# Performance work log

Measured on AMD Instinct MI355X. Metric: run time of the kernel, lower is better.

The kernel has to match this reference:

```python
import jax, jax.numpy as jnp
import numpy as np

DIM = 1024; SD = 1024; N_BANDS = 4; MIMO_P = 8; BATCH = 2; L = 2048
LOG10000 = float(np.log(10000.0))


def _hippo_freqs(sd):
    n = jnp.arange(sd, dtype=jnp.float32)
    f = jnp.sqrt(2.0 * n + 1.0)
    f = f / f[-1]
    return jnp.exp(-f * LOG10000)


def setup_inputs() -> dict:
    key = jax.random.key(0)
    ks = jax.random.split(key, 16)
    dim, sd = DIM, SD
    wscale = 1.0 / np.sqrt(dim)
    n = jnp.arange(sd, dtype=jnp.float32)
    b0 = jnp.sqrt(2.0 * n + 1.0); b0 = b0 / b0[-1]
    b0_inv = jnp.log(jnp.expm1(jnp.clip(b0, 1e-6, None)))  # softplus^-1 of hippo b
    G = sd // MIMO_P
    inp = dict(
        x=jax.random.normal(ks[0], (BATCH, L, dim), jnp.float32),
        z_prev=jax.random.normal(ks[1], (BATCH, L, dim), jnp.float32),
        W_psi=jax.random.normal(ks[2], (2 * sd, dim), jnp.float32) * wscale,
        b_psi=jnp.zeros(2 * sd, jnp.float32),
        W_phi=jax.random.normal(ks[3], (2 * sd, dim), jnp.float32) * wscale,
        b_phi=jnp.zeros(2 * sd, jnp.float32),
        W_gate=jax.random.normal(ks[4], (1, dim), jnp.float32) * wscale,
        b_gate=jnp.zeros(1, jnp.float32),
        surprise_gain=jnp.zeros(1, jnp.float32),
        omega=_hippo_freqs(sd),
        log_gamma=jax.random.normal(ks[5], (sd,), jnp.float32) * 0.5 - 7.0,
        dt=jnp.float32(np.log(np.expm1(0.1))),  # layer_idx=0, depth=1 -> target_dt=0.1
        W_bs=jax.random.normal(ks[6], (sd, dim), jnp.float32) * 0.02,
        b_bs=b0_inv,
        W_ps=jax.random.uniform(ks[7], (sd, dim), jnp.float32, -wscale, wscale),
        b_ps=jnp.zeros(sd, jnp.float32),
        W_btx=jax.random.normal(ks[8], (sd, dim), jnp.float32) * 0.02,
        b_btx=b0_inv,
        W_bth=jax.random.normal(ks[9], (sd, 2 * sd), jnp.float32) * 0.02,
        b_bth=jnp.zeros(sd, jnp.float32),
        W_ptx=jax.random.uniform(ks[10], (sd, dim), jnp.float32, -wscale, wscale),
        b_ptx=jnp.zeros(sd, jnp.float32),
        mimo_w=jnp.eye(MIMO_P, dtype=jnp.float32)[None].repeat(G, 0)
               + 0.02 * jax.random.normal(ks[11], (G, MIMO_P, MIMO_P), jnp.float32),
        tau=jnp.ones(1, jnp.float32),
        beta=jnp.zeros(1, jnp.float32),
    )
    return inp


def _forward(x, z_prev, W_psi, b_psi, W_phi, b_phi, W_gate, b_gate, surprise_gain,
             omega, log_gamma, dt, W_bs, b_bs, W_ps, b_ps, W_btx, b_btx,
             W_bth, b_bth, W_ptx, b_ptx, mimo_w, tau, beta):
    Bsz, Ls, D = x.shape
    sd = omega.shape[0]
    n_fft = 1 << (2 * Ls - 1).bit_length()  # static

    # unitary mask: band 0 = lowest hippo frequencies (slowest modes) stay lossless
    freqs = _hippo_freqs(sd)
    order = jnp.argsort(freqs)
    band0 = order[: sd // N_BANDS]
    not_unitary = jnp.ones(sd, jnp.float32).at[band0].set(0.0)

    lin = lambda a, W, bb: a @ W.T + bb

    psi_raw = lin(x, W_psi, b_psi)
    psi = jax.lax.complex(psi_raw[..., :sd], psi_raw[..., sd:])
    phi_raw = lin(x, W_phi, b_phi)
    phi = jax.lax.complex(phi_raw[..., :sd], phi_raw[..., sd:])

    gate = jax.nn.sigmoid(lin(x, W_gate, b_gate))  # [B,L,1]
    surprise = jnp.mean(jnp.abs(x - z_prev), -1, keepdims=True)
    gate = gate * (1.0 + jnp.tanh(surprise_gain) * surprise)

    dt_eff = jax.nn.softplus(dt)
    gamma_eff = jax.nn.softplus(log_gamma) * not_unitary
    lam = jax.lax.complex(-gamma_eff, omega)  # [SD]
    t = jnp.arange(Ls, dtype=jnp.float32)
    kernel_raw = jnp.exp(lam[None, :] * (t[:, None] * dt_eff))  # [L,SD] A^t
    k_pad = jnp.concatenate([jnp.zeros((2, sd), kernel_raw.dtype), kernel_raw], 0)
    kernel_simpson = (k_pad[2:] + 4.0 * k_pad[1:-1] + k_pad[:-2]) / 6.0  # Simpson taps

    Kf_scout = jnp.fft.fft(kernel_raw.T, n=n_fft, axis=1)      # [SD,n_fft]
    Kf_true = jnp.fft.fft(kernel_simpson.T, n=n_fft, axis=1)

    def fftconv(U, Kf):  # causal conv via FFT: U [B,L,SD] complex
        Uf = jnp.fft.fft(jnp.transpose(U, (0, 2, 1)), n=n_fft, axis=2)
        H = jnp.fft.ifft(Uf * Kf[None], axis=2)[:, :, :Ls]
        return jnp.transpose(H, (0, 2, 1))

    # ---- scout wave: input-only LTI ----
    b_scout = jax.nn.softplus(lin(x, W_bs, b_bs))
    ph_s = jnp.pi * jnp.tanh(lin(x, W_ps, b_ps))
    Bc_s = jax.lax.complex(b_scout * jnp.cos(ph_s), b_scout * jnp.sin(ph_s))
    U_scout = gate * Bc_s * psi
    H_scout = fftconv(U_scout, Kf_scout)
    H_prev = jnp.pad(H_scout, ((0, 0), (1, 0), (0, 0)))[:, :-1]  # shift by 1
    scout_rms = jnp.sqrt(jnp.mean(H_prev.real ** 2 + H_prev.imag ** 2, -1, keepdims=True) + 1e-6)
    Hn = H_prev / scout_rms
    H_flat = jnp.concatenate([Hn.real, Hn.imag], -1)  # [B,L,2SD]

    # ---- true wave: state-dependent B, Simpson quadrature kernel ----
    b_true = jax.nn.softplus(lin(x, W_btx, b_btx) + lin(H_flat, W_bth, b_bth))
    ph_t = jnp.pi * jnp.tanh(lin(x, W_ptx, b_ptx))
    Bc_t = jax.lax.complex(b_true * jnp.cos(ph_t), b_true * jnp.sin(ph_t))
    U_true = gate * Bc_t * psi
    H = fftconv(U_true, Kf_true)

    read_rms = jnp.sqrt(jnp.mean(H.real ** 2 + H.imag ** 2, -1, keepdims=True) + 1e-6)
    Hn2 = H / read_rms

    # block-diagonal MIMO mixing in groups of mimo_p
    G = sd // MIMO_P
    Hg = Hn2.reshape(Bsz, Ls, G, MIMO_P)
    Hm = jnp.einsum('blgp,gpq->blgq', Hg, mimo_w.astype(Hg.dtype)).reshape(Bsz, Ls, sd)

    # Born-rule measurement: out = Re(h * phi^*), affine read temperature
    out = jnp.real(Hm * jnp.conj(phi))
    return tau * out + beta  # SD == dim -> out_proj is Identity


def reference(x, z_prev, W_psi, b_psi, W_phi, b_phi, W_gate, b_gate, surprise_gain,
              omega, log_gamma, dt, W_bs, b_bs, W_ps, b_ps, W_btx, b_btx,
              W_bth, b_bth, W_ptx, b_ptx, mimo_w, tau, beta):
    return _forward(x, z_prev, W_psi, b_psi, W_phi, b_phi, W_gate, b_gate,
                    surprise_gain, omega, log_gamma, dt, W_bs, b_bs, W_ps, b_ps,
                    W_btx, b_btx, W_bth, b_bth, W_ptx, b_ptx, mimo_w, tau, beta)
```

## Files before the change

### kernel.cpp

```cpp
#include <hip/hip_runtime.h>
#include <math.h>

#define DIMX   1024
#define SDN    1024
#define BATCHN 2
#define LSEQ   2048
#define BLROWS (BATCHN*LSEQ)
#define NCHUNK 128
#define LCHUNK (LSEQ/NCHUNK)
#define PI_F   3.14159265358979f

typedef unsigned short ushort_t;
typedef unsigned int uint_t;
typedef __bf16 bf16_t;
typedef bf16_t bf16x8 __attribute__((ext_vector_type(8)));
typedef float f32x4 __attribute__((ext_vector_type(4)));

__device__ __forceinline__ ushort_t f2bf_rne(float f) {
  unsigned u = __float_as_uint(f);
  u = u + 0x7fffu + ((u >> 16) & 1u);
  return (ushort_t)(u >> 16);
}

__device__ __forceinline__ float bf2f(ushort_t u) {
  return __uint_as_float(((unsigned)u) << 16);
}

__device__ __forceinline__ uint_t pk2(float2 v) {
  return (uint_t)f2bf_rne(v.x) | ((uint_t)f2bf_rne(v.y) << 16);
}
__device__ __forceinline__ float2 upk2(uint_t u) {
  return make_float2(__uint_as_float(u << 16), __uint_as_float(u & 0xffff0000u));
}

__device__ __forceinline__ float2 cfma2(float2 a, float2 v, float2 u) {
  float re = fmaf(a.x, v.x, fmaf(-a.y, v.y, u.x));
  float im = fmaf(a.x, v.y, fmaf(a.y, v.x, u.y));
  return make_float2(re, im);
}
__device__ __forceinline__ float2 cmul2(float2 a, float2 b) {
  return make_float2(a.x * b.x - a.y * b.y, a.x * b.y + a.y * b.x);
}

__device__ __forceinline__ float fast_softplus(float x) {
  return x > 15.f ? x : __logf(1.f + __expf(x));
}
__device__ __forceinline__ float fast_tanh(float x) {
  float xc = fminf(fmaxf(x, -9.f), 9.f);
  float t = __expf(2.f * xc);
  return (t - 1.f) * __builtin_amdgcn_rcpf(t + 1.f);
}

__device__ __forceinline__ void gload_lds16(const ushort_t* g, ushort_t* l) {
  __builtin_amdgcn_global_load_lds(
      (const __attribute__((address_space(1))) void*)g,
      (__attribute__((address_space(3))) void*)l, 16, 0, 0);
}

__global__ __launch_bounds__(256) void prep_kernel(
    const float* __restrict__ x, const float* __restrict__ z_prev,
    const float* __restrict__ Wpsi, const float* __restrict__ Wphi,
    const float* __restrict__ Wbs, const float* __restrict__ Wps,
    const float* __restrict__ Wbtx, const float* __restrict__ Wptx,
    const float* __restrict__ Wbth,
    const float* __restrict__ b_psi, const float* __restrict__ b_phi,
    const float* __restrict__ b_bs, const float* __restrict__ b_ps,
    const float* __restrict__ b_btx, const float* __restrict__ b_ptx,
    const float* __restrict__ Wg, const float* __restrict__ bg,
    const float* __restrict__ sg,
    const float* __restrict__ omega, const float* __restrict__ log_gamma,
    const float* __restrict__ dt,
    ushort_t* __restrict__ xb, ushort_t* __restrict__ wcat,
    ushort_t* __restrict__ wbthb, float* __restrict__ bcat,
    float* __restrict__ gate, float2* __restrict__ a_out,
    float2* __restrict__ A_out) {
  int b = blockIdx.x;
  int tid = threadIdx.x;
  if (b < 4096) {
    int i = tid * 4;
    const float* xp = x + (size_t)b * DIMX;
    const float* zp = z_prev + (size_t)b * DIMX;
    float4 xv = *(const float4*)(xp + i);
    float4 zv = *(const float4*)(zp + i);
    float4 wv = *(const float4*)(Wg + i);
    ushort4 o;
    o.x = f2bf_rne(xv.x); o.y = f2bf_rne(xv.y);
    o.z = f2bf_rne(xv.z); o.w = f2bf_rne(xv.w);
    *(ushort4*)(xb + (size_t)b * DIMX + i) = o;
    float dot = xv.x * wv.x + xv.y * wv.y + xv.z * wv.z + xv.w * wv.w;
    float sur = fabsf(xv.x - zv.x) + fabsf(xv.y - zv.y) +
                fabsf(xv.z - zv.z) + fabsf(xv.w - zv.w);
    __shared__ float sdot[256], ssur[256];
    sdot[tid] = dot; ssur[tid] = sur;
    __syncthreads();
    for (int o_ = 128; o_ > 0; o_ >>= 1) {
      if (tid < o_) { sdot[tid] += sdot[tid + o_]; ssur[tid] += ssur[tid + o_]; }
      __syncthreads();
    }
    if (tid == 0) {
      float gs = 1.f / (1.f + expf(-(sdot[0] + bg[0])));
      gate[b] = gs * (1.f + tanhf(sg[0]) * (ssur[0] * (1.f / DIMX)));
    }
    return;
  }
  b -= 4096;
  if (b < 10240) {
    const float* src; ushort_t* dst; int off;
    if (b < 2048)       { src = Wpsi; dst = wcat;             off = b; }
    else if (b < 4096)  { src = Wphi; dst = wcat + 2097152u;  off = b - 2048; }
    else if (b < 5120)  { src = Wbs;  dst = wcat + 4194304u;  off = b - 4096; }
    else if (b < 6144)  { src = Wps;  dst = wcat + 5242880u;  off = b - 5120; }
    else if (b < 7168)  { src = Wbtx; dst = wcat + 6291456u;  off = b - 6144; }
    else if (b < 8192)  { src = Wptx; dst = wcat + 7340032u;  off = b - 7168; }
    else                { src = Wbth; dst = wbthb;            off = b - 8192; }
    int i = (off * 256 + tid) * 4;
    float4 v = *(const float4*)(src + i);
    ushort4 o;
    o.x = f2bf_rne(v.x); o.y = f2bf_rne(v.y);
    o.z = f2bf_rne(v.z); o.w = f2bf_rne(v.w);
    *(ushort4*)(dst + i) = o;
    return;
  }
  b -= 10240;
  if (b < 32) {
    int n = b * 256 + tid;
    float v;
    if (n < 2048) v = b_psi[n];
    else if (n < 4096) v = b_phi[n - 2048];
    else if (n < 5120) v = b_bs[n - 4096];
    else if (n < 6144) v = b_ps[n - 5120];
    else if (n < 7168) v = b_btx[n - 6144];
    else v = b_ptx[n - 7168];
    bcat[n] = v;
    return;
  }
  int s = (b - 32) * 256 + tid;
  double dtv = (double)dt[0];
  double dte = dtv > 20.0 ? dtv : log1p(exp(dtv));
  double gam = 0.0;
  if (s < SDN - SDN / 4) {
    double lg = (double)log_gamma[s];
    gam = lg > 20.0 ? lg : log1p(exp(lg));
  }
  double th = (double)omega[s] * dte;
  double r  = exp(-gam * dte);
  a_out[s] = make_float2((float)(r * cos(th)), (float)(r * sin(th)));
  double thl = th * (double)LCHUNK;
  double rl  = exp(-gam * dte * (double)LCHUNK);
  A_out[s] = make_float2((float)(rl * cos(thl)), (float)(rl * sin(thl)));
}

template<int MODE>
__global__ __launch_bounds__(256, 2) void gemm_bf16(
    const ushort_t* __restrict__ Xb, const ushort_t* __restrict__ Wb,
    const float* __restrict__ bias, ushort_t* __restrict__ Cb) {
  __shared__ ushort_t As[2][4096];
  __shared__ ushort_t Bs[2][4096];
  const int tid = threadIdx.x;
  const int w = tid >> 6, l = tid & 63;
  int bm, bn, ldx, ldw;
  const ushort_t *Xp, *Wp;
  if (MODE == 0) {
    int b = blockIdx.x;
    int xcd = b & 7, idx = b >> 3;
    int tx = ((xcd & 3) << 4) + (idx & 15);
    int ty = ((xcd >> 2) << 4) + (idx >> 4);
    bm = ty << 7; bn = tx << 7;
    ldx = 1024; ldw = 1024;
    Xp = Xb; Wp = Wb;
  } else {
    bm = blockIdx.y << 7; bn = blockIdx.x << 7;
    ldx = 2048; ldw = 2048;
    Xp = Xb + blockIdx.z * 1024;
    Wp = Wb + blockIdx.z * 1024;
  }
  const int wr = w >> 1, wc = w & 1;

  const int srow = tid >> 2;
  const int c8 = (((tid & 3) - (tid >> 3)) & 3) << 3;
  const ushort_t* ga0 = Xp + (size_t)(bm + srow) * ldx + c8;
  const ushort_t* ga1 = Xp + (size_t)(bm + 64 + srow) * ldx + c8;
  const ushort_t* gb0 = Wp + (size_t)(bn + srow) * ldw + c8;
  const ushort_t* gb1 = Wp + (size_t)(bn + 64 + srow) * ldw + c8;

  f32x4 acc[4][4] = {};
  const int nk = 32;

#define STAGE(buf, kt)                                   \
  do {                                                   \
    gload_lds16(ga0 + (kt), &As[buf][w * 512]);          \
    gload_lds16(ga1 + (kt), &As[buf][2048 + w * 512]);   \
    gload_lds16(gb0 + (kt), &Bs[buf][w * 512]);          \
    gload_lds16(gb1 + (kt), &Bs[buf][2048 + w * 512]);   \
  } while (0)

  STAGE(0, 0);
  __syncthreads();

  const int rl = l & 15, kh = l >> 4;
  const int chunkp = (kh + (rl >> 1)) & 3;
  for (int kt = 0; kt < nk; ++kt) {
    int cur = kt & 1;
    if (kt + 1 < nk) STAGE(cur ^ 1, (kt + 1) * 32);
    const uint4* Af = (const uint4*)As[cur];
    const uint4* Bf = (const uint4*)Bs[cur];
    bf16x8 a[4], b[4];
#pragma unroll
    for (int i = 0; i < 4; ++i)
      a[i] = __builtin_bit_cast(bf16x8, Af[(wr * 64 + i * 16 + rl) * 4 + chunkp]);
#pragma unroll
    for (int j = 0; j < 4; ++j)
      b[j] = __builtin_bit_cast(bf16x8, Bf[(wc * 64 + j * 16 + rl) * 4 + chunkp]);
#pragma unroll
    for (int i = 0; i < 4; ++i)
#pragma unroll
      for (int j = 0; j < 4; ++j)
        acc[i][j] = __builtin_amdgcn_mfma_f32_16x16x32_bf16(a[i], b[j], acc[i][j], 0, 0, 0);
    __syncthreads();
  }
#undef STAGE

#pragma unroll
  for (int i = 0; i < 4; ++i) {
    int mrow = bm + wr * 64 + i * 16 + (l >> 4) * 4;
#pragma unroll
    for (int j = 0; j < 4; ++j) {
      int ncol = bn + wc * 64 + j * 16 + (l & 15);
      if (MODE == 0) {
        float bv = bias[ncol];
#pragma unroll
        for (int r = 0; r < 4; ++r)
          Cb[(size_t)(mrow + r) * 8192 + ncol] = f2bf_rne(acc[i][j][r] + bv);
      } else {
        ushort_t* P = Cb + (size_t)blockIdx.z * (4096u * 1024u);
#pragma unroll
        for (int r = 0; r < 4; ++r)
          P[(size_t)(mrow + r) * 1024 + ncol] = f2bf_rne(acc[i][j][r]);
      }
    }
  }
}


__global__ __launch_bounds__(256) void u_scout(
    const float* __restrict__ gate, const ushort_t* __restrict__ proj,
    uint_t* __restrict__ U) {
  int idx2 = blockIdx.x * 256 + threadIdx.x;
  int m = idx2 >> 9, sp = (idx2 & 511) << 1;
  const ushort_t* pr = proj + ((size_t)m << 13);
  float g = gate[m];
  uint_t bsu = *(const uint_t*)(pr + 4096 + sp);
  uint_t psu = *(const uint_t*)(pr + 5120 + sp);
  uint_t pre = *(const uint_t*)(pr + sp);
  uint_t pim = *(const uint_t*)(pr + 1024 + sp);
  uint_t o[2];
#pragma unroll
  for (int e = 0; e < 2; ++e) {
    float bv = fast_softplus(bf2f((ushort_t)(e ? (bsu >> 16) : (bsu & 0xffff))));
    float ph = PI_F * fast_tanh(bf2f((ushort_t)(e ? (psu >> 16) : (psu & 0xffff))));
    float sph, cph;
    __sincosf(ph, &sph, &cph);
    float br = bv * cph, bi = bv * sph;
    float prf = bf2f((ushort_t)(e ? (pre >> 16) : (pre & 0xffff)));
    float pif = bf2f((ushort_t)(e ? (pim >> 16) : (pim & 0xffff)));
    o[e] = pk2(make_float2(g * (br * prf - bi * pif), g * (br * pif + bi * prf)));
  }
  *(uint2*)(U + ((size_t)m << 10) + sp) = make_uint2(o[0], o[1]);
}

__global__ __launch_bounds__(256) void u_true(
    const float* __restrict__ gate, const ushort_t* __restrict__ proj,
    const ushort_t* __restrict__ P0, const ushort_t* __restrict__ P1,
    const float* __restrict__ b_bth, uint_t* __restrict__ U) {
  int idx2 = blockIdx.x * 256 + threadIdx.x;
  int m = idx2 >> 9, sp = (idx2 & 511) << 1;
  const ushort_t* pr = proj + ((size_t)m << 13);
  float g = gate[m];
  size_t base = ((size_t)m << 10) + sp;
  uint_t btu = *(const uint_t*)(pr + 6144 + sp);
  uint_t ptu = *(const uint_t*)(pr + 7168 + sp);
  uint_t p0u = *(const uint_t*)(P0 + base);
  uint_t p1u = *(const uint_t*)(P1 + base);
  float2 bb = *(const float2*)(b_bth + sp);
  uint_t pre = *(const uint_t*)(pr + sp);
  uint_t pim = *(const uint_t*)(pr + 1024 + sp);
  uint_t o[2];
#pragma unroll
  for (int e = 0; e < 2; ++e) {
    float blv = bf2f((ushort_t)(e ? (btu >> 16) : (btu & 0xffff)))
              + bf2f((ushort_t)(e ? (p0u >> 16) : (p0u & 0xffff)))
              + bf2f((ushort_t)(e ? (p1u >> 16) : (p1u & 0xffff)))
              + (e ? bb.y : bb.x);
    float bv = fast_softplus(blv);
    float ph = PI_F * fast_tanh(bf2f((ushort_t)(e ? (ptu >> 16) : (ptu & 0xffff))));
    float sph, cph;
    __sincosf(ph, &sph, &cph);
    float br = bv * cph, bi = bv * sph;
    float prf = bf2f((ushort_t)(e ? (pre >> 16) : (pre & 0xffff)));
    float pif = bf2f((ushort_t)(e ? (pim >> 16) : (pim & 0xffff)));
    o[e] = pk2(make_float2(g * (br * prf - bi * pif), g * (br * pif + bi * prf)));
  }
  *(uint2*)(U + base) = make_uint2(o[0], o[1]);
}

__global__ __launch_bounds__(256) void scan_stage1(
    const uint_t* __restrict__ U, const float2* __restrict__ a,
    float2* __restrict__ carry) {
  int s = blockIdx.x * 256 + threadIdx.x;
  int c = blockIdx.y, b = blockIdx.z;
  float2 av = a[s];
  float2 V = make_float2(0.f, 0.f);
  const uint_t* Up = U + (size_t)(b * LSEQ + c * LCHUNK) * SDN + s;
#pragma unroll 8
  for (int t = 0; t < LCHUNK; ++t)
    V = cfma2(av, V, upk2(Up[(size_t)t * SDN]));
  carry[(size_t)(b * NCHUNK + c) * SDN + s] = V;
}

__global__ __launch_bounds__(256) void scan_stage2(
    const float2* __restrict__ carry, const float2* __restrict__ Ac,
    float2* __restrict__ prefix) {
  int tid = threadIdx.x;
  int lane = tid & 63;
  int s = blockIdx.x * 4 + (tid >> 6);
  int b = blockIdx.z;
  float2 Av = Ac[s];
  size_t base0 = (size_t)(b * NCHUNK + 2 * lane) * SDN + s;
  float2 c0 = carry[base0];
  float2 c1 = carry[base0 + SDN];
  float2 x = cfma2(Av, c0, c1);
  float2 M = cmul2(Av, Av);
#pragma unroll
  for (int sh = 1; sh < 64; sh <<= 1) {
    float2 y;
    y.x = __shfl_up(x.x, sh, 64);
    y.y = __shfl_up(x.y, sh, 64);
    if (lane >= sh) x = cfma2(M, y, x);
    M = cmul2(M, M);
  }
  float2 p0;
  p0.x = __shfl_up(x.x, 1, 64);
  p0.y = __shfl_up(x.y, 1, 64);
  if (lane == 0) p0 = make_float2(0.f, 0.f);
  float2 p1 = cfma2(Av, p0, c0);
  prefix[base0] = p0;
  prefix[base0 + SDN] = p1;
}

__global__ __launch_bounds__(256) void scan_stage3(
    const uint_t* __restrict__ U, const float2* __restrict__ a,
    const float2* __restrict__ prefix, uint_t* __restrict__ Vout) {
  int s = blockIdx.x * 256 + threadIdx.x;
  int c = blockIdx.y, b = blockIdx.z;
  float2 av = a[s];
  float2 V = prefix[(size_t)(b * NCHUNK + c) * SDN + s];
  size_t base = (size_t)(b * LSEQ + c * LCHUNK) * SDN + s;
#pragma unroll 8
  for (int t = 0; t < LCHUNK; ++t) {
    V = cfma2(av, V, upk2(U[base + (size_t)t * SDN]));
    Vout[base + (size_t)t * SDN] = pk2(V);
  }
}

__global__ __launch_bounds__(256) void hflat_kernel(
    const uint_t* __restrict__ V, ushort_t* __restrict__ Hflat) {
  int m = blockIdx.x;
  int t = m & (LSEQ - 1);
  float2 v[4];
  float sum = 0.f;
#pragma unroll
  for (int i = 0; i < 4; ++i) {
    int s = threadIdx.x + i * 256;
    float2 vv = make_float2(0.f, 0.f);
    if (t > 0) vv = upk2(V[(size_t)(m - 1) * SDN + s]);
    v[i] = vv;
    sum += vv.x * vv.x + vv.y * vv.y;
  }
  __shared__ float red[256];
  red[threadIdx.x] = sum;
  __syncthreads();
  for (int o = 128; o > 0; o >>= 1) {
    if (threadIdx.x < o) red[threadIdx.x] += red[threadIdx.x + o];
    __syncthreads();
  }
  float inv = 1.0f / sqrtf(red[0] * (1.f / SDN) + 1e-6f);
  ushort_t* hr = Hflat + ((size_t)m << 11);
#pragma unroll
  for (int i = 0; i < 4; ++i) {
    int s = threadIdx.x + i * 256;
    hr[s] = f2bf_rne(v[i].x * inv);
    hr[SDN + s] = f2bf_rne(v[i].y * inv);
  }
}

__global__ __launch_bounds__(256) void final_kernel(
    const uint_t* __restrict__ V, const ushort_t* __restrict__ proj,
    const float* __restrict__ mimo, const float* __restrict__ tau,
    const float* __restrict__ beta, float* __restrict__ out) {
  int bid = blockIdx.x;
  int m = ((bid & 7) << 9) | (bid >> 3);
  int t = m & (LSEQ - 1);
  __shared__ float2 hl[SDN];
  __shared__ float red[256];
  float sum = 0.f;
#pragma unroll
  for (int i = 0; i < 4; ++i) {
    int s = threadIdx.x + i * 256;
    float2 v0 = upk2(V[(size_t)m * SDN + s]);
    float2 v1 = make_float2(0.f, 0.f), v2 = make_float2(0.f, 0.f);
    if (t >= 1) v1 = upk2(V[(size_t)(m - 1) * SDN + s]);
    if (t >= 2) v2 = upk2(V[(size_t)(m - 2) * SDN + s]);
    float2 h = make_float2((v0.x + 4.f * v1.x + v2.x) * (1.f / 6.f),
                           (v0.y + 4.f * v1.y + v2.y) * (1.f / 6.f));
    hl[s] = h;
    sum += h.x * h.x + h.y * h.y;
  }
  red[threadIdx.x] = sum;
  __syncthreads();
  for (int o = 128; o > 0; o >>= 1) {
    if (threadIdx.x < o) red[threadIdx.x] += red[threadIdx.x + o];
    __syncthreads();
  }
  float inv = 1.0f / sqrtf(red[0] * (1.f / SDN) + 1e-6f);
  float tv = tau[0], bv = beta[0];
  const ushort_t* pp = proj + ((size_t)m << 13) + 2048;
#pragma unroll
  for (int i = 0; i < 4; ++i) {
    int s = threadIdx.x + i * 256;
    int g = s >> 3, q = s & 7;
    const float* wp = mimo + (size_t)g * 64 + q;
    float hr = 0.f, hi = 0.f;
#pragma unroll
    for (int p = 0; p < 8; ++p) {
      float wv = wp[p * 8];
      float2 hp = hl[(g << 3) + p];
      hr = fmaf(hp.x, wv, hr);
      hi = fmaf(hp.y, wv, hi);
    }
    hr *= inv; hi *= inv;
    float o1 = hr * bf2f(pp[s]) + hi * bf2f(pp[SDN + s]);
    out[(size_t)m * SDN + s] = tv * o1 + bv;
  }
}

extern "C" void kernel_launch(void* const* d_in, const int* in_sizes, int n_in,
                              void* d_out, int out_size, void* d_ws, size_t ws_size,
                              hipStream_t stream) {
  const float* x      = (const float*)d_in[0];
  const float* z_prev = (const float*)d_in[1];
  const float* W_psi  = (const float*)d_in[2];
  const float* b_psi  = (const float*)d_in[3];
  const float* W_phi  = (const float*)d_in[4];
  const float* b_phi  = (const float*)d_in[5];
  const float* W_gate = (const float*)d_in[6];
  const float* b_gate = (const float*)d_in[7];
  const float* s_gain = (const float*)d_in[8];
  const float* omega  = (const float*)d_in[9];
  const float* log_g  = (const float*)d_in[10];
  const float* dt     = (const float*)d_in[11];
  const float* W_bs   = (const float*)d_in[12];
  const float* b_bs   = (const float*)d_in[13];
  const float* W_ps   = (const float*)d_in[14];
  const float* b_ps   = (const float*)d_in[15];
  const float* W_btx  = (const float*)d_in[16];
  const float* b_btx  = (const float*)d_in[17];
  const float* W_bth  = (const float*)d_in[18];
  const float* b_bth  = (const float*)d_in[19];
  const float* W_ptx  = (const float*)d_in[20];
  const float* b_ptx  = (const float*)d_in[21];
  const float* mimo_w = (const float*)d_in[22];
  const float* tau    = (const float*)d_in[23];
  const float* beta   = (const float*)d_in[24];
  float* out = (float*)d_out;

  float* ws = (float*)d_ws;
  const size_t M1 = 1 << 20;
  ushort_t* proj   = (ushort_t*)ws;
  uint_t*   U      = (uint_t*)(ws + 16 * M1);
  uint_t*   V      = U;
  ushort_t* xb     = (ushort_t*)(ws + 24 * M1);
  ushort_t* wcat   = (ushort_t*)(ws + 26 * M1);
  ushort_t* P0     = wcat;
  ushort_t* P1     = wcat + 4u * 1024u * 1024u;
  ushort_t* wbthb  = (ushort_t*)(ws + 30 * M1);
  ushort_t* hflatB = (ushort_t*)(ws + 31 * M1);
  float*    bcat   = ws + 35 * M1;
  float*    gate   = bcat + 8192;
  float2*   ac     = (float2*)(gate + 4096);
  float2*   Ac     = ac + 1024;
  float2*   carry  = Ac + 1024;
  float2*   prefix = carry + 262144;
  (void)ws_size; (void)in_sizes; (void)n_in; (void)out_size;

  dim3 blk(256);
  dim3 sgrid(SDN / 256, NCHUNK, BATCHN);
  dim3 s2grid(SDN / 4, 1, BATCHN);

  prep_kernel<<<dim3(14372), blk, 0, stream>>>(
      x, z_prev, W_psi, W_phi, W_bs, W_ps, W_btx, W_ptx, W_bth,
      b_psi, b_phi, b_bs, b_ps, b_btx, b_ptx,
      W_gate, b_gate, s_gain, omega, log_g, dt,
      xb, wcat, wbthb, bcat, gate, ac, Ac);

  gemm_bf16<0><<<dim3(2048), blk, 0, stream>>>(xb, wcat, bcat, proj);

  u_scout<<<dim3(BLROWS * SDN / 512), blk, 0, stream>>>(gate, proj, U);
  scan_stage1<<<sgrid, blk, 0, stream>>>(U, ac, carry);
  scan_stage2<<<s2grid, blk, 0, stream>>>(carry, Ac, prefix);
  scan_stage3<<<sgrid, blk, 0, stream>>>(U, ac, prefix, V);

  hflat_kernel<<<dim3(BLROWS), blk, 0, stream>>>(V, hflatB);
  gemm_bf16<1><<<dim3(8, 32, 2), blk, 0, stream>>>(hflatB, wbthb, bcat, P0);

  u_true<<<dim3(BLROWS * SDN / 512), blk, 0, stream>>>(gate, proj, P0, P1, b_bth, U);
  scan_stage1<<<sgrid, blk, 0, stream>>>(U, ac, carry);
  scan_stage2<<<s2grid, blk, 0, stream>>>(carry, Ac, prefix);
  scan_stage3<<<sgrid, blk, 0, stream>>>(U, ac, prefix, V);

  final_kernel<<<dim3(BLROWS), blk, 0, stream>>>(V, proj, mimo_w, tau, beta, out);
}
```

Baseline: 202.5 us.

## Fuse three-stage chunked scan into one cooperative kernel with grid syncs

Replaces the three separate scan kernels (chunk carry, carry prefix, chunk rescan) with a single cooperative launch that uses grid-wide barriers between the phases. The middle phase reuses the first 512 blocks of the same grid. This removes two kernel launches and their inter-kernel gaps per scan, of which there are two in the forward pass. The grid is 1024 blocks of 256 threads, which must all be co-resident for the cooperative launch, and grid.sync adds its own barrier cost.

```diff
diff --git a/kernel.cpp b/kernel.cpp
--- a/kernel.cpp
+++ b/kernel.cpp
@@ -1,5 +1,8 @@
 #include <hip/hip_runtime.h>
+#include <hip/hip_cooperative_groups.h>
 #include <math.h>
+
+namespace cg = cooperative_groups;
 
 #define DIMX   1024
 #define SDN    1024
@@ -303,62 +306,62 @@
   *(uint2*)(U + base) = make_uint2(o[0], o[1]);
 }
 
-__global__ __launch_bounds__(256) void scan_stage1(
-    const uint_t* __restrict__ U, const float2* __restrict__ a,
-    float2* __restrict__ carry) {
-  int s = blockIdx.x * 256 + threadIdx.x;
-  int c = blockIdx.y, b = blockIdx.z;
-  float2 av = a[s];
-  float2 V = make_float2(0.f, 0.f);
-  const uint_t* Up = U + (size_t)(b * LSEQ + c * LCHUNK) * SDN + s;
+__global__ __launch_bounds__(256) void scan_fused(
+    uint_t* __restrict__ U, const float2* __restrict__ a,
+    const float2* __restrict__ Ac, float2* __restrict__ carry,
+    float2* __restrict__ prefix) {
+  cg::grid_group grid = cg::this_grid();
+  const int tid = threadIdx.x;
+  const int s = blockIdx.x * 256 + tid;
+  const int c = blockIdx.y, b = blockIdx.z;
+  const float2 av = a[s];
+  {
+    float2 V = make_float2(0.f, 0.f);
+    const uint_t* Up = U + (size_t)(b * LSEQ + c * LCHUNK) * SDN + s;
 #pragma unroll 8
-  for (int t = 0; t < LCHUNK; ++t)
-    V = cfma2(av, V, upk2(Up[(size_t)t * SDN]));
-  carry[(size_t)(b * NCHUNK + c) * SDN + s] = V;
-}
-
-__global__ __launch_bounds__(256) void scan_stage2(
-    const float2* __restrict__ carry, const float2* __restrict__ Ac,
-    float2* __restrict__ prefix) {
-  int tid = threadIdx.x;
-  int lane = tid & 63;
-  int s = blockIdx.x * 4 + (tid >> 6);
-  int b = blockIdx.z;
-  float2 Av = Ac[s];
-  size_t base0 = (size_t)(b * NCHUNK + 2 * lane) * SDN + s;
-  float2 c0 = carry[base0];
-  float2 c1 = carry[base0 + SDN];
-  float2 x = cfma2(Av, c0, c1);
-  float2 M = cmul2(Av, Av);
-#pragma unroll
-  for (int sh = 1; sh < 64; sh <<= 1) {
-    float2 y;
-    y.x = __shfl_up(x.x, sh, 64);
-    y.y = __shfl_up(x.y, sh, 64);
-    if (lane >= sh) x = cfma2(M, y, x);
-    M = cmul2(M, M);
-  }
-  float2 p0;
-  p0.x = __shfl_up(x.x, 1, 64);
-  p0.y = __shfl_up(x.y, 1, 64);
-  if (lane == 0) p0 = make_float2(0.f, 0.f);
-  float2 p1 = cfma2(Av, p0, c0);
-  prefix[base0] = p0;
-  prefix[base0 + SDN] = p1;
-}
-
-__global__ __launch_bounds__(256) void scan_stage3(
-    const uint_t* __restrict__ U, const float2* __restrict__ a,
-    const float2* __restrict__ prefix, uint_t* __restrict__ Vout) {
-  int s = blockIdx.x * 256 + threadIdx.x;
-  int c = blockIdx.y, b = blockIdx.z;
-  float2 av = a[s];
-  float2 V = prefix[(size_t)(b * NCHUNK + c) * SDN + s];
-  size_t base = (size_t)(b * LSEQ + c * LCHUNK) * SDN + s;
+    for (int t = 0; t < LCHUNK; ++t)
+      V = cfma2(av, V, upk2(Up[(size_t)t * SDN]));
+    carry[(size_t)(b * NCHUNK + c) * SDN + s] = V;
+  }
+  grid.sync();
+  {
+    int fid = (blockIdx.z * NCHUNK + blockIdx.y) * (SDN / 256) + blockIdx.x;
+    if (fid < 512) {
+      int lane = tid & 63;
+      int s2 = (fid & 255) * 4 + (tid >> 6);
+      int b2 = fid >> 8;
+      float2 Av = Ac[s2];
+      size_t base0 = (size_t)(b2 * NCHUNK + 2 * lane) * SDN + s2;
+      float2 c0 = carry[base0];
+      float2 c1 = carry[base0 + SDN];
+      float2 x = cfma2(Av, c0, c1);
+      float2 M = cmul2(Av, Av);
+#pragma unroll
+      for (int sh = 1; sh < 64; sh <<= 1) {
+        float2 y;
+        y.x = __shfl_up(x.x, sh, 64);
+        y.y = __shfl_up(x.y, sh, 64);
+        if (lane >= sh) x = cfma2(M, y, x);
+        M = cmul2(M, M);
+      }
+      float2 p0;
+      p0.x = __shfl_up(x.x, 1, 64);
+      p0.y = __shfl_up(x.y, 1, 64);
+      if (lane == 0) p0 = make_float2(0.f, 0.f);
+      float2 p1 = cfma2(Av, p0, c0);
+      prefix[base0] = p0;
+      prefix[base0 + SDN] = p1;
+    }
+  }
+  grid.sync();
+  {
+    float2 V = prefix[(size_t)(b * NCHUNK + c) * SDN + s];
+    size_t base = (size_t)(b * LSEQ + c * LCHUNK) * SDN + s;
 #pragma unroll 8
-  for (int t = 0; t < LCHUNK; ++t) {
-    V = cfma2(av, V, upk2(U[base + (size_t)t * SDN]));
-    Vout[base + (size_t)t * SDN] = pk2(V);
+    for (int t = 0; t < LCHUNK; ++t) {
+      V = cfma2(av, V, upk2(U[base + (size_t)t * SDN]));
+      U[base + (size_t)t * SDN] = pk2(V);
+    }
   }
 }
 
@@ -494,7 +497,13 @@
 
   dim3 blk(256);
   dim3 sgrid(SDN / 256, NCHUNK, BATCHN);
-  dim3 s2grid(SDN / 4, 1, BATCHN);
+
+  uint_t*       sc_U  = U;
+  const float2* sc_a  = ac;
+  const float2* sc_Ac = Ac;
+  float2*       sc_c  = carry;
+  float2*       sc_p  = prefix;
+  void* sargs[5] = {&sc_U, &sc_a, &sc_Ac, &sc_c, &sc_p};
 
   prep_kernel<<<dim3(14372), blk, 0, stream>>>(
       x, z_prev, W_psi, W_phi, W_bs, W_ps, W_btx, W_ptx, W_bth,
@@ -505,17 +514,13 @@
   gemm_bf16<0><<<dim3(2048), blk, 0, stream>>>(xb, wcat, bcat, proj);
 
   u_scout<<<dim3(BLROWS * SDN / 512), blk, 0, stream>>>(gate, proj, U);
-  scan_stage1<<<sgrid, blk, 0, stream>>>(U, ac, carry);
-  scan_stage2<<<s2grid, blk, 0, stream>>>(carry, Ac, prefix);
-  scan_stage3<<<sgrid, blk, 0, stream>>>(U, ac, prefix, V);
+  hipLaunchCooperativeKernel((void*)scan_fused, sgrid, blk, sargs, 0, stream);
 
   hflat_kernel<<<dim3(BLROWS), blk, 0, stream>>>(V, hflatB);
   gemm_bf16<1><<<dim3(8, 32, 2), blk, 0, stream>>>(hflatB, wbthb, bcat, P0);
 
   u_true<<<dim3(BLROWS * SDN / 512), blk, 0, stream>>>(gate, proj, P0, P1, b_bth, U);
-  scan_stage1<<<sgrid, blk, 0, stream>>>(U, ac, carry);
-  scan_stage2<<<s2grid, blk, 0, stream>>>(carry, Ac, prefix);
-  scan_stage3<<<sgrid, blk, 0, stream>>>(U, ac, prefix, V);
+  hipLaunchCooperativeKernel((void*)scan_fused, sgrid, blk, sargs, 0, stream);
 
   final_kernel<<<dim3(BLROWS), blk, 0, stream>>>(V, proj, mimo_w, tau, beta, out);
 }
```

Result: slower. 550.8 us (+172.1%).
